# Performance work log

Hardware: AMD Instinct MI355X
Metric: run time of the kernel (lower is better)

Reference implementation:

```python
import jax, jax.numpy as jnp
import numpy as np

B, S, IN, H, OUT = 4096, 32, 256, 128, 256


def setup_inputs() -> dict:
    key = jax.random.key(0)
    k = jax.random.split(key, 5)
    x = jax.random.normal(k[0], (B, S, IN), dtype=jnp.float32)
    # Stacked per-subband weights: torch nn.Linear computes x @ W.T + b;
    # here we store W already transposed as [S, in, out].
    W1 = jax.random.normal(k[1], (S, IN, H), dtype=jnp.float32) * (1.0 / np.sqrt(IN))
    b1 = jax.random.normal(k[2], (S, H), dtype=jnp.float32) * 0.01
    W2 = jax.random.normal(k[3], (S, H, OUT), dtype=jnp.float32) * (1.0 / np.sqrt(H))
    b2 = jax.random.normal(k[4], (S, OUT), dtype=jnp.float32) * 0.01
    return {"x": x, "W1": W1, "b1": b1, "W2": W2, "b2": b2}


def reference(x, W1, b1, W2, b2):
    # All subbands fused into one batched GEMM + ReLU + batched GEMM.
    # h: [B, S, H]
    h = jax.nn.relu(jnp.einsum('bsi,sih->bsh', x, W1) + b1)
    # out: [B, S, OUT]
    out = jnp.einsum('bsh,sho->bso', h, W2) + b2
    return out
```

## Files before the change

### kernel.cpp

```cpp
#include <hip/hip_runtime.h>
#include <hip/hip_bf16.h>

#define B_   4096
#define S_   32
#define IN_  256
#define H_   128
#define OUT_ 256

typedef __attribute__((ext_vector_type(8))) short bf16x8;
typedef __attribute__((ext_vector_type(4))) float f32x4;
typedef unsigned long long ull;

__device__ __forceinline__ unsigned short f2bf(float f) {
    union { float f; unsigned u; } v; v.f = f;
    unsigned r = v.u + 0x7FFFu + ((v.u >> 16) & 1u);
    return (unsigned short)(r >> 16);
}
__device__ __forceinline__ unsigned cvt_pk(float lo, float hi) {
    unsigned r;
    asm("v_cvt_pk_bf16_f32 %0, %1, %2" : "=v"(r) : "v"(lo), "v"(hi));
    return r;
}

__global__ __launch_bounds__(256) void pack_both(const float* __restrict__ W1,
                                                 const float* __restrict__ W2,
                                                 unsigned short* __restrict__ w1f,
                                                 unsigned short* __restrict__ w2f) {
    __shared__ float tile[32][257];
    const int bid = blockIdx.x;
    const int t = threadIdx.x;
    if (bid < 256) {
        const int s = bid >> 3, kk = bid & 7;
#pragma unroll
        for (int i = 0; i < 16; ++i) {
            int idx = t + i * 256;
            int kl = idx >> 7, h = idx & 127;
            tile[kl][h] = W1[((size_t)s * IN_ + kk * 32 + kl) * H_ + h];
        }
        __syncthreads();
#pragma unroll
        for (int rep = 0; rep < 2; ++rep) {
            int idx = t + rep * 256;
            int hf = idx >> 6, l = idx & 63, l15 = l & 15, l4 = l >> 4;
            unsigned short o8[8];
#pragma unroll
            for (int j = 0; j < 8; ++j) o8[j] = f2bf(tile[l4 * 8 + j][hf * 16 + l15]);
            *(bf16x8*)(w1f + (((size_t)(s * 8 + kk) * 8 + hf) * 64 + l) * 8) = *(bf16x8*)o8;
        }
    } else {
        const int rel = bid - 256, s = rel >> 2, kkh = rel & 3;
#pragma unroll
        for (int i = 0; i < 32; ++i) {
            int idx = t + i * 256;
            int kl = idx >> 8, o = idx & 255;
            tile[kl][o] = W2[((size_t)s * H_ + kkh * 32 + kl) * OUT_ + o];
        }
        __syncthreads();
#pragma unroll
        for (int rep = 0; rep < 4; ++rep) {
            int idx = t + rep * 256;
            int g = idx >> 6, l = idx & 63, l15 = l & 15, l4 = l >> 4;
            unsigned short o8[8];
#pragma unroll
            for (int j = 0; j < 8; ++j) o8[j] = f2bf(tile[l4 * 8 + j][g * 16 + l15]);
            *(bf16x8*)(w2f + (((size_t)(s * 16 + g) * 4 + kkh) * 64 + l) * 8) = *(bf16x8*)o8;
        }
    }
}

__global__ __launch_bounds__(768) void subband_fused_kernel(
        const float* __restrict__ x,
        const unsigned short* __restrict__ w1f,
        const unsigned short* __restrict__ w2f,
        const float* __restrict__ b1,
        const float* __restrict__ b2,
        float* __restrict__ out) {
    __shared__ __align__(16) unsigned char lds[161280];
    unsigned char* w1l = lds;
    unsigned char* w2l = lds + 65536;
    unsigned char* repb = lds + 126976;
    float* b1l = (float*)(lds + 159744);
    float* b2l = (float*)(lds + 160256);

    const int bid = blockIdx.x;
    const int s     = bid >> 3;
    const int chunk = bid & 7;
    const int tid = threadIdx.x;
    const int w = tid >> 6, l = tid & 63, l15 = l & 15, l4 = l >> 4;
    unsigned char* rep = repb + w * 2048;

#define LDG(dst, p) asm volatile("global_load_dwordx4 %0, %1, off" : "=v"(dst) : "v"(p))
#define WAITV0                                                                   \
    asm volatile("s_waitcnt vmcnt(0)"                                            \
        : "+v"(v[0]), "+v"(v[1]), "+v"(v[2]), "+v"(v[3]),                        \
          "+v"(v[4]), "+v"(v[5]), "+v"(v[6]), "+v"(v[7]),                        \
          "+v"(v[8]), "+v"(v[9]), "+v"(v[10]), "+v"(v[11]),                      \
          "+v"(v[12]), "+v"(v[13]), "+v"(v[14]), "+v"(v[15]) :: "memory")
#define ISSUE_X(ROW0)                                                            \
    do {                                                                         \
        const float* xr_ = x + ((size_t)((ROW0) + l15) * S_ + s) * IN_ + l4 * 8; \
        _Pragma("unroll")                                                        \
        for (int kk = 0; kk < 8; ++kk) {                                         \
            LDG(v[2 * kk],     xr_ + kk * 32);                                   \
            LDG(v[2 * kk + 1], xr_ + kk * 32 + 4);                               \
        }                                                                        \
    } while (0)

    f32x4 v[16];
    ISSUE_X(chunk * 512 + w * 16);

    const unsigned char* w1src = (const unsigned char*)(w1f + (size_t)s * 32768);
#pragma unroll
    for (int i = 0; i < 5; ++i)
        *(bf16x8*)(w1l + tid * 16 + i * 12288) = *(const bf16x8*)(w1src + tid * 16 + i * 12288);
    if (tid < 256)
        *(bf16x8*)(w1l + tid * 16 + 61440) = *(const bf16x8*)(w1src + tid * 16 + 61440);
    const unsigned char* w2src = (const unsigned char*)(w2f + (size_t)s * 32768);
#pragma unroll
    for (int i = 0; i < 5; ++i)
        *(bf16x8*)(w2l + tid * 16 + i * 12288) = *(const bf16x8*)(w2src + tid * 16 + i * 12288);

    bf16x8 w2r[4];
#pragma unroll
    for (int kkh = 0; kkh < 4; ++kkh)
        w2r[kkh] = *(const bf16x8*)(w2src + (((size_t)15 * 4 + kkh) * 64 + l) * 16);

    if (tid < 128)      b1l[tid]       = b1[s * H_ + tid];
    else if (tid < 384) b2l[tid - 128] = b2[s * OUT_ + (tid - 128)];

    __syncthreads();

#pragma unroll 1
    for (int r = 0; r < 3; ++r) {
        const int tile = r * 12 + w;
        if (tile >= 32) continue;
        const int rowt = chunk * 512 + tile * 16;

        WAITV0;
        __builtin_amdgcn_sched_barrier(0);

        bf16x8 xb[8];
#pragma unroll
        for (int kk = 0; kk < 8; ++kk) {
            union { unsigned u[4]; bf16x8 b; } p;
            p.u[0] = cvt_pk(v[2 * kk][0],     v[2 * kk][1]);
            p.u[1] = cvt_pk(v[2 * kk][2],     v[2 * kk][3]);
            p.u[2] = cvt_pk(v[2 * kk + 1][0], v[2 * kk + 1][1]);
            p.u[3] = cvt_pk(v[2 * kk + 1][2], v[2 * kk + 1][3]);
            xb[kk] = p.b;
        }

        {
            const int ntile = (r + 1) * 12 + w;
            if (r < 2 && ntile < 32) ISSUE_X(chunk * 512 + ntile * 16);
        }

        f32x4 acc1[8];
#pragma unroll
        for (int hf = 0; hf < 8; ++hf) {
            const float4 bv = *(const float4*)(b1l + hf * 16 + l4 * 4);
            acc1[hf][0] = bv.x; acc1[hf][1] = bv.y; acc1[hf][2] = bv.z; acc1[hf][3] = bv.w;
        }
        __builtin_amdgcn_s_setprio(1);
#pragma unroll
        for (int kk = 0; kk < 8; ++kk)
#pragma unroll
            for (int hf = 0; hf < 8; ++hf) {
                const bf16x8 wf = *(const bf16x8*)(w1l + ((kk * 8 + hf) * 64 + l) * 16);
                acc1[hf] = __builtin_amdgcn_mfma_f32_16x16x32_bf16(wf, xb[kk], acc1[hf], 0, 0, 0);
            }
        __builtin_amdgcn_s_setprio(0);

        bf16x8 hfr[4];
#pragma unroll
        for (int half = 0; half < 2; ++half) {
#pragma unroll
            for (int hh = 0; hh < 4; ++hh) {
                const int hf = half * 4 + hh;
                unsigned p0 = cvt_pk(fmaxf(acc1[hf][0], 0.f), fmaxf(acc1[hf][1], 0.f));
                unsigned p1 = cvt_pk(fmaxf(acc1[hf][2], 0.f), fmaxf(acc1[hf][3], 0.f));
                ull p = (ull)p0 | ((ull)p1 << 32);
                const int loc = (hf >> 1) & 1;
                const int l4p = ((hf & 1) << 1) | (l4 >> 1);
                *(ull*)(rep + loc * 1024 + (l4p * 16 + l15) * 16 + ((l4 & 1) * 8)) = p;
            }
            asm volatile("s_waitcnt lgkmcnt(0)" ::: "memory");
            __builtin_amdgcn_sched_barrier(0);
            hfr[half * 2 + 0] = *(const bf16x8*)(rep + l * 16);
            hfr[half * 2 + 1] = *(const bf16x8*)(rep + 1024 + l * 16);
            asm volatile("s_waitcnt lgkmcnt(0)" ::: "memory");
            __builtin_amdgcn_sched_barrier(0);
        }

        float* op = out + ((size_t)(rowt + l15) * S_ + s) * OUT_;
#pragma unroll
        for (int g = 0; g < 16; ++g) {
            const float4 bv = *(const float4*)(b2l + g * 16 + l4 * 4);
            f32x4 acc2;
            acc2[0] = bv.x; acc2[1] = bv.y; acc2[2] = bv.z; acc2[3] = bv.w;
            __builtin_amdgcn_s_setprio(1);
#pragma unroll
            for (int kkh = 0; kkh < 4; ++kkh) {
                const bf16x8 wf = (g < 15)
                    ? *(const bf16x8*)(w2l + ((g * 4 + kkh) * 64 + l) * 16)
                    : w2r[kkh];
                acc2 = __builtin_amdgcn_mfma_f32_16x16x32_bf16(wf, hfr[kkh], acc2, 0, 0, 0);
            }
            __builtin_amdgcn_s_setprio(0);
            *(f32x4*)(op + g * 16 + l4 * 4) = acc2;
        }
    }
#undef ISSUE_X
#undef WAITV0
#undef LDG
}

extern "C" void kernel_launch(void* const* d_in, const int* in_sizes, int n_in,
                              void* d_out, int out_size, void* d_ws, size_t ws_size,
                              hipStream_t stream) {
    const float* x  = (const float*)d_in[0];
    const float* W1 = (const float*)d_in[1];
    const float* b1 = (const float*)d_in[2];
    const float* W2 = (const float*)d_in[3];
    const float* b2 = (const float*)d_in[4];
    float* out = (float*)d_out;

    unsigned short* w1f = (unsigned short*)d_ws;
    unsigned short* w2f = w1f + (size_t)S_ * 8 * 8 * 64 * 8;

    pack_both<<<384, 256, 0, stream>>>(W1, W2, w1f, w2f);
    subband_fused_kernel<<<256, 768, 0, stream>>>(x, w1f, w2f, b1, b2, out);
}
```

Before: 68.23 us.

## Process two 16-row tiles per wave to reuse LDS weight fragments

Each wave now handles a pair of 16-row tiles (32 rows) per iteration, so every W1/W2 fragment read from LDS feeds two MFMAs instead of one. The loop count drops from three to two rounds of 12 waves over 16 pairs. The goal is to halve LDS weight traffic per MFMA. In exchange, accumulator and register pressure roughly doubles, and the x prefetch overlap is weaker: the second tile's load is issued and waited on back-to-back inside the iteration, and the next pair's prefetch is issued only after GEMM1. Fewer waves have work in the second round, which leaves some load imbalance.

```diff
diff --git a/kernel.cpp b/kernel.cpp
--- a/kernel.cpp
+++ b/kernel.cpp
@@ -105,9 +105,43 @@
             LDG(v[2 * kk + 1], xr_ + kk * 32 + 4);                               \
         }                                                                        \
     } while (0)
+#define CVT_XB(XB)                                                               \
+    do {                                                                         \
+        _Pragma("unroll")                                                        \
+        for (int kk = 0; kk < 8; ++kk) {                                         \
+            union { unsigned u[4]; bf16x8 b; } p;                                \
+            p.u[0] = cvt_pk(v[2 * kk][0],     v[2 * kk][1]);                     \
+            p.u[1] = cvt_pk(v[2 * kk][2],     v[2 * kk][3]);                     \
+            p.u[2] = cvt_pk(v[2 * kk + 1][0], v[2 * kk + 1][1]);                 \
+            p.u[3] = cvt_pk(v[2 * kk + 1][2], v[2 * kk + 1][3]);                 \
+            XB[kk] = p.b;                                                        \
+        }                                                                        \
+    } while (0)
+#define REPACK2(ACC, HFR)                                                        \
+    do {                                                                         \
+        _Pragma("unroll")                                                        \
+        for (int half = 0; half < 2; ++half) {                                   \
+            _Pragma("unroll")                                                    \
+            for (int hh = 0; hh < 4; ++hh) {                                     \
+                const int hf = half * 4 + hh;                                    \
+                unsigned p0 = cvt_pk(fmaxf(ACC[hf][0], 0.f), fmaxf(ACC[hf][1], 0.f)); \
+                unsigned p1 = cvt_pk(fmaxf(ACC[hf][2], 0.f), fmaxf(ACC[hf][3], 0.f)); \
+                ull p = (ull)p0 | ((ull)p1 << 32);                               \
+                const int loc = (hf >> 1) & 1;                                   \
+                const int l4p = ((hf & 1) << 1) | (l4 >> 1);                     \
+                *(ull*)(rep + loc * 1024 + (l4p * 16 + l15) * 16 + ((l4 & 1) * 8)) = p; \
+            }                                                                    \
+            asm volatile("s_waitcnt lgkmcnt(0)" ::: "memory");                   \
+            __builtin_amdgcn_sched_barrier(0);                                   \
+            HFR[half * 2 + 0] = *(const bf16x8*)(rep + l * 16);                  \
+            HFR[half * 2 + 1] = *(const bf16x8*)(rep + 1024 + l * 16);           \
+            asm volatile("s_waitcnt lgkmcnt(0)" ::: "memory");                   \
+            __builtin_amdgcn_sched_barrier(0);                                   \
+        }                                                                        \
+    } while (0)
 
     f32x4 v[16];
-    ISSUE_X(chunk * 512 + w * 16);
+    ISSUE_X(chunk * 512 + w * 32);
 
     const unsigned char* w1src = (const unsigned char*)(w1f + (size_t)s * 32768);
 #pragma unroll
@@ -131,35 +165,27 @@
     __syncthreads();
 
 #pragma unroll 1
-    for (int r = 0; r < 3; ++r) {
-        const int tile = r * 12 + w;
-        if (tile >= 32) continue;
-        const int rowt = chunk * 512 + tile * 16;
+    for (int r = 0; r < 2; ++r) {
+        const int pair = r * 12 + w;
+        if (pair >= 16) continue;
+        const int rowp = chunk * 512 + pair * 32;
 
         WAITV0;
         __builtin_amdgcn_sched_barrier(0);
-
-        bf16x8 xb[8];
-#pragma unroll
-        for (int kk = 0; kk < 8; ++kk) {
-            union { unsigned u[4]; bf16x8 b; } p;
-            p.u[0] = cvt_pk(v[2 * kk][0],     v[2 * kk][1]);
-            p.u[1] = cvt_pk(v[2 * kk][2],     v[2 * kk][3]);
-            p.u[2] = cvt_pk(v[2 * kk + 1][0], v[2 * kk + 1][1]);
-            p.u[3] = cvt_pk(v[2 * kk + 1][2], v[2 * kk + 1][3]);
-            xb[kk] = p.b;
-        }
-
-        {
-            const int ntile = (r + 1) * 12 + w;
-            if (r < 2 && ntile < 32) ISSUE_X(chunk * 512 + ntile * 16);
-        }
-
-        f32x4 acc1[8];
+        bf16x8 xbA[8], xbB[8];
+        CVT_XB(xbA);
+        ISSUE_X(rowp + 16);
+        WAITV0;
+        __builtin_amdgcn_sched_barrier(0);
+        CVT_XB(xbB);
+
+        f32x4 acc1A[8], acc1B[8];
 #pragma unroll
         for (int hf = 0; hf < 8; ++hf) {
             const float4 bv = *(const float4*)(b1l + hf * 16 + l4 * 4);
-            acc1[hf][0] = bv.x; acc1[hf][1] = bv.y; acc1[hf][2] = bv.z; acc1[hf][3] = bv.w;
+            acc1A[hf][0] = bv.x; acc1A[hf][1] = bv.y;
+            acc1A[hf][2] = bv.z; acc1A[hf][3] = bv.w;
+            acc1B[hf] = acc1A[hf];
         }
         __builtin_amdgcn_s_setprio(1);
 #pragma unroll
@@ -167,49 +193,44 @@
 #pragma unroll
             for (int hf = 0; hf < 8; ++hf) {
                 const bf16x8 wf = *(const bf16x8*)(w1l + ((kk * 8 + hf) * 64 + l) * 16);
-                acc1[hf] = __builtin_amdgcn_mfma_f32_16x16x32_bf16(wf, xb[kk], acc1[hf], 0, 0, 0);
+                acc1A[hf] = __builtin_amdgcn_mfma_f32_16x16x32_bf16(wf, xbA[kk], acc1A[hf], 0, 0, 0);
+                acc1B[hf] = __builtin_amdgcn_mfma_f32_16x16x32_bf16(wf, xbB[kk], acc1B[hf], 0, 0, 0);
             }
         __builtin_amdgcn_s_setprio(0);
 
-        bf16x8 hfr[4];
-#pragma unroll
-        for (int half = 0; half < 2; ++half) {
-#pragma unroll
-            for (int hh = 0; hh < 4; ++hh) {
-                const int hf = half * 4 + hh;
-                unsigned p0 = cvt_pk(fmaxf(acc1[hf][0], 0.f), fmaxf(acc1[hf][1], 0.f));
-                unsigned p1 = cvt_pk(fmaxf(acc1[hf][2], 0.f), fmaxf(acc1[hf][3], 0.f));
-                ull p = (ull)p0 | ((ull)p1 << 32);
-                const int loc = (hf >> 1) & 1;
-                const int l4p = ((hf & 1) << 1) | (l4 >> 1);
-                *(ull*)(rep + loc * 1024 + (l4p * 16 + l15) * 16 + ((l4 & 1) * 8)) = p;
-            }
-            asm volatile("s_waitcnt lgkmcnt(0)" ::: "memory");
-            __builtin_amdgcn_sched_barrier(0);
-            hfr[half * 2 + 0] = *(const bf16x8*)(rep + l * 16);
-            hfr[half * 2 + 1] = *(const bf16x8*)(rep + 1024 + l * 16);
-            asm volatile("s_waitcnt lgkmcnt(0)" ::: "memory");
-            __builtin_amdgcn_sched_barrier(0);
-        }
-
-        float* op = out + ((size_t)(rowt + l15) * S_ + s) * OUT_;
+        bf16x8 hfrA[4], hfrB[4];
+        REPACK2(acc1A, hfrA);
+        REPACK2(acc1B, hfrB);
+
+        {
+            const int npair = (r + 1) * 12 + w;
+            if (r < 1 && npair < 16) ISSUE_X(chunk * 512 + npair * 32);
+        }
+
+        float* opA = out + ((size_t)(rowp + l15) * S_ + s) * OUT_;
+        float* opB = opA + (size_t)16 * S_ * OUT_;
 #pragma unroll
         for (int g = 0; g < 16; ++g) {
             const float4 bv = *(const float4*)(b2l + g * 16 + l4 * 4);
-            f32x4 acc2;
-            acc2[0] = bv.x; acc2[1] = bv.y; acc2[2] = bv.z; acc2[3] = bv.w;
+            f32x4 accA, accB;
+            accA[0] = bv.x; accA[1] = bv.y; accA[2] = bv.z; accA[3] = bv.w;
+            accB = accA;
             __builtin_amdgcn_s_setprio(1);
 #pragma unroll
             for (int kkh = 0; kkh < 4; ++kkh) {
                 const bf16x8 wf = (g < 15)
                     ? *(const bf16x8*)(w2l + ((g * 4 + kkh) * 64 + l) * 16)
                     : w2r[kkh];
-                acc2 = __builtin_amdgcn_mfma_f32_16x16x32_bf16(wf, hfr[kkh], acc2, 0, 0, 0);
+                accA = __builtin_amdgcn_mfma_f32_16x16x32_bf16(wf, hfrA[kkh], accA, 0, 0, 0);
+                accB = __builtin_amdgcn_mfma_f32_16x16x32_bf16(wf, hfrB[kkh], accB, 0, 0, 0);
             }
             __builtin_amdgcn_s_setprio(0);
-            *(f32x4*)(op + g * 16 + l4 * 4) = acc2;
+            *(f32x4*)(opA + g * 16 + l4 * 4) = accA;
+            *(f32x4*)(opB + g * 16 + l4 * 4) = accB;
         }
     }
+#undef REPACK2
+#undef CVT_XB
 #undef ISSUE_X
 #undef WAITV0
 #undef LDG
```

New measurement: 110.5 us. 61.9% more time.
